# Optimization experiments

Measured on AMD Instinct MI355X. Metric: run time of the kernel, lower is better.

The kernel has to match this reference:

```python
import jax, jax.numpy as jnp
import numpy as np

VOCAB = 267735
CUTOFFS = [20000, 40000, 200000, VOCAB]  # self.cutoffs (incl. vocab)
SHORTLIST = 20000
N_CLUSTERS = 3


def setup_inputs() -> dict:
    key = jax.random.key(0)
    ks = jax.random.split(key, 16)
    s = 0.02  # init scale as in reset_parameters / linear_weight_init
    return {
        "x": jax.random.normal(ks[0], (1024, 1024), jnp.float32),
        "target": jax.random.randint(ks[1], (1024,), 0, VOCAB, jnp.int64),
        "W0": s * jax.random.normal(ks[2], (20000, 1024), jnp.float32),
        "b0": jnp.zeros((20000,), jnp.float32),
        "W1": s * jax.random.normal(ks[3], (20000, 256), jnp.float32),
        "b1": jnp.zeros((20000,), jnp.float32),
        "W2": s * jax.random.normal(ks[4], (160000, 64), jnp.float32),
        "b2": jnp.zeros((160000,), jnp.float32),
        "W3": s * jax.random.normal(ks[5], (67735, 16), jnp.float32),
        "b3": jnp.zeros((67735,), jnp.float32),
        "cluster_weight": s * jax.random.normal(ks[6], (3, 1024), jnp.float32),
        "cluster_bias": jnp.zeros((3,), jnp.float32),
        "P0": s * jax.random.normal(ks[7], (1024, 1024), jnp.float32),
        "P1": s * jax.random.normal(ks[8], (1024, 256), jnp.float32),
        "P2": s * jax.random.normal(ks[9], (1024, 64), jnp.float32),
        "P3": s * jax.random.normal(ks[10], (1024, 16), jnp.float32),
    }


def _logits(x, P, W, b):
    # F.linear(hidden, proj.t()) == x @ proj ; then F.linear(proj_hid, W, b)
    return (x @ P) @ W.T + b


def reference(x, target, W0, b0, W1, b1, W2, b2, W3, b3,
              cluster_weight, cluster_bias, P0, P1, P2, P3):
    N = x.shape[0]
    # head: shortlist + cluster logits
    head_w = jnp.concatenate([W0, cluster_weight], axis=0)  # [20003, 1024]
    head_b = jnp.concatenate([b0, cluster_bias], axis=0)
    head_logp = jax.nn.log_softmax(_logits(x, P0, head_w, head_b), axis=-1)

    # remap targets falling in tail clusters to their cluster token in the head
    # cluster idx -> head index SHORTLIST + N_CLUSTERS - 1 - idx
    head_idx = target
    for idx in range(N_CLUSTERS):
        l, r = CUTOFFS[idx], CUTOFFS[idx + 1]
        in_c = (target >= l) & (target < r)
        head_idx = jnp.where(in_c, SHORTLIST + N_CLUSTERS - 1 - idx, head_idx)

    nll = -jnp.take_along_axis(head_logp, head_idx[:, None], axis=1)[:, 0]

    # tail clusters: dense masked cross-entropy (same math as gather/scatter
    # version: each token contributes only its own cluster's CE)
    tails = [(W1, b1, P1), (W2, b2, P2), (W3, b3, P3)]
    for idx, (W, b, P) in enumerate(tails):
        l, r = CUTOFFS[idx], CUTOFFS[idx + 1]
        mask = (target >= l) & (target < r)
        t = jnp.clip(target - l, 0, r - l - 1)
        logp = jax.nn.log_softmax(_logits(x, P, W, b), axis=-1)  # [N, r-l]
        ce = -jnp.take_along_axis(logp, t[:, None], axis=1)[:, 0]
        nll = nll + jnp.where(mask, ce, jnp.zeros_like(ce))
    return nll
```

## Files before the change

### kernel.cpp

```cpp
#include <hip/hip_runtime.h>
#include <hip/hip_bf16.h>
#include <math.h>


typedef __attribute__((ext_vector_type(4))) float f32x4;
typedef __attribute__((ext_vector_type(8))) short bf16x8;
typedef __attribute__((ext_vector_type(8))) unsigned short ushort8;

#define NEG_INF (-INFINITY)

static __device__ __forceinline__ unsigned short f2b(float f) {
  unsigned u = __builtin_bit_cast(unsigned, f);
  u += 0x7fffu + ((u >> 16) & 1u);
  return (unsigned short)(u >> 16);
}
static __device__ __forceinline__ f32x4 zero4() { f32x4 z = {0.f,0.f,0.f,0.f}; return z; }
static __device__ __forceinline__ ushort8 zero8() { ushort8 z = {0,0,0,0,0,0,0,0}; return z; }

__global__ __launch_bounds__(512, 2)
void gemm_proj(const float* __restrict__ A, const unsigned short* __restrict__ B,
               int V, int K,
               float* __restrict__ Cf, unsigned short* __restrict__ Cb)
{
  __shared__ unsigned short As[256 * 40];
  __shared__ unsigned short Bs[128 * 40];

  const int t = threadIdx.x;
  const int rowBase = blockIdx.y * 256;
  const int colBase = blockIdx.x * 128;

  const int ar = t >> 1, ak = (t & 1) << 4;
  const int br = t >> 2, bk = (t & 3) << 3;
  const bool bval = (colBase + br) < V;
  const size_t arow = (size_t)(rowBase + ar) * K;
  const size_t brow = (size_t)(colBase + br) * K;

  f32x4 aS[4]; ushort8 bSb;
  auto LOAD = [&](int k0) {
    #pragma unroll
    for (int i = 0; i < 4; ++i) aS[i] = *(const f32x4*)(A + arow + k0 + ak + i * 4);
    bSb = bval ? *(const ushort8*)(B + brow + k0 + bk) : zero8();
  };
  auto STORE = [&]() {
    ushort8 p0, p1;
    #pragma unroll
    for (int j = 0; j < 4; ++j) {
      p0[j] = f2b(aS[0][j]); p0[j + 4] = f2b(aS[1][j]);
      p1[j] = f2b(aS[2][j]); p1[j + 4] = f2b(aS[3][j]);
    }
    *(ushort8*)&As[ar * 40 + ak]     = p0;
    *(ushort8*)&As[ar * 40 + ak + 8] = p1;
    *(ushort8*)&Bs[br * 40 + bk] = bSb;
  };

  const int lane = t & 63, w = t >> 6;
  const int wr = w >> 1, wc = w & 1;
  const int g = lane >> 4, fr = lane & 15;

  f32x4 acc[4][4];
  #pragma unroll
  for (int m = 0; m < 4; ++m)
    #pragma unroll
    for (int n = 0; n < 4; ++n) acc[m][n] = zero4();

  LOAD(0);
  for (int k0 = 0; k0 < K; k0 += 32) {
    __syncthreads();
    STORE();
    __syncthreads();
    if (k0 + 32 < K) LOAD(k0 + 32);
    bf16x8 af[4], bf[4];
    #pragma unroll
    for (int m = 0; m < 4; ++m)
      af[m] = *(const bf16x8*)&As[(wr * 64 + m * 16 + fr) * 40 + g * 8];
    #pragma unroll
    for (int n = 0; n < 4; ++n)
      bf[n] = *(const bf16x8*)&Bs[(wc * 64 + n * 16 + fr) * 40 + g * 8];
    #pragma unroll
    for (int m = 0; m < 4; ++m)
      #pragma unroll
      for (int n = 0; n < 4; ++n)
        acc[m][n] = __builtin_amdgcn_mfma_f32_16x16x32_bf16(af[m], bf[n], acc[m][n], 0, 0, 0);
  }

  #pragma unroll
  for (int m = 0; m < 4; ++m) {
    int row = rowBase + wr * 64 + m * 16 + g * 4;
    #pragma unroll
    for (int n = 0; n < 4; ++n) {
      int col = colBase + wc * 64 + n * 16 + fr;
      if (col < V) {
        #pragma unroll
        for (int r = 0; r < 4; ++r) {
          float v = acc[m][n][r];
          Cf[(size_t)(row + r) * V + col] = v;
          Cb[(size_t)(row + r) * V + col] = f2b(v);
        }
      }
    }
  }
}

__global__ __launch_bounds__(512, 2)
void gemm_lse_big(const unsigned short* __restrict__ A, const float* __restrict__ B,
                  const float* __restrict__ bias, int V, int K, int T,
                  float* __restrict__ parts)
{
  __shared__ unsigned short As[256 * 40];
  __shared__ unsigned short Bs[128 * 40];
  __shared__ float red[2][256];

  const int t = threadIdx.x;
  const int rowBase = blockIdx.y * 256;
  const int strip = blockIdx.x;
  const int KS = K >> 5;

  const int ar = t >> 1, ak = (t & 1) << 4;
  const int br = t >> 2, bk = (t & 3) << 3;
  const size_t arow = (size_t)(rowBase + ar) * K;

  ushort8 aSb[2]; f32x4 bS[2];
  auto LOADA = [&](int k0) {
    aSb[0] = *(const ushort8*)(A + arow + k0 + ak);
    aSb[1] = *(const ushort8*)(A + arow + k0 + ak + 8);
  };
  auto LOADB = [&](int tile, int k0) {
    size_t row = (size_t)(strip * T + tile) * 128 + br;
    bool v = row < (size_t)V;
    bS[0] = v ? *(const f32x4*)(B + row * K + k0 + bk)     : zero4();
    bS[1] = v ? *(const f32x4*)(B + row * K + k0 + bk + 4) : zero4();
  };
  auto STORE = [&]() {
    *(ushort8*)&As[ar * 40 + ak]     = aSb[0];
    *(ushort8*)&As[ar * 40 + ak + 8] = aSb[1];
    ushort8 pb;
    #pragma unroll
    for (int j = 0; j < 4; ++j) { pb[j] = f2b(bS[0][j]); pb[j + 4] = f2b(bS[1][j]); }
    *(ushort8*)&Bs[br * 40 + bk] = pb;
  };

  const int lane = t & 63, w = t >> 6;
  const int wr = w >> 1, wc = w & 1;
  const int g = lane >> 4, fr = lane & 15;

  float S[4][4];
  #pragma unroll
  for (int m = 0; m < 4; ++m)
    #pragma unroll
    for (int r = 0; r < 4; ++r) S[m][r] = 0.f;
  f32x4 acc[4][4];
  #pragma unroll
  for (int m = 0; m < 4; ++m)
    #pragma unroll
    for (int n = 0; n < 4; ++n) acc[m][n] = zero4();

  float bcol[4];
  LOADA(0); LOADB(0, 0);
  int tile = 0, ks = 0;
  const int total = T * KS;
  for (int step = 0; step < total; ++step) {
    __syncthreads();
    STORE();
    __syncthreads();
    if (ks == 0) {
      #pragma unroll
      for (int n = 0; n < 4; ++n) {
        int col = (strip * T + tile) * 128 + wc * 64 + n * 16 + fr;
        bcol[n] = (col < V) ? bias[col] : NEG_INF;
      }
    }
    const bool last = (ks == KS - 1);
    int nt = tile, nk = ks + 1;
    if (nk == KS) { nk = 0; nt++; }
    if (nt < T) { LOADA(nk * 32); LOADB(nt, nk * 32); }
    bf16x8 af[4], bfr[4];
    #pragma unroll
    for (int m = 0; m < 4; ++m)
      af[m] = *(const bf16x8*)&As[(wr * 64 + m * 16 + fr) * 40 + g * 8];
    #pragma unroll
    for (int n = 0; n < 4; ++n)
      bfr[n] = *(const bf16x8*)&Bs[(wc * 64 + n * 16 + fr) * 40 + g * 8];
    #pragma unroll
    for (int m = 0; m < 4; ++m)
      #pragma unroll
      for (int n = 0; n < 4; ++n)
        acc[m][n] = __builtin_amdgcn_mfma_f32_16x16x32_bf16(af[m], bfr[n], acc[m][n], 0, 0, 0);
    if (last) {
      #pragma unroll
      for (int m = 0; m < 4; ++m)
        #pragma unroll
        for (int n = 0; n < 4; ++n)
          #pragma unroll
          for (int r = 0; r < 4; ++r)
            S[m][r] += __expf(acc[m][n][r] + bcol[n]);
      #pragma unroll
      for (int m = 0; m < 4; ++m)
        #pragma unroll
        for (int n = 0; n < 4; ++n) acc[m][n] = zero4();
    }
    tile = nt; ks = nk;
  }

  #pragma unroll
  for (int off = 1; off <= 8; off <<= 1)
    #pragma unroll
    for (int m = 0; m < 4; ++m)
      #pragma unroll
      for (int r = 0; r < 4; ++r) S[m][r] += __shfl_xor(S[m][r], off, 64);
  if (fr == 0) {
    #pragma unroll
    for (int m = 0; m < 4; ++m)
      #pragma unroll
      for (int r = 0; r < 4; ++r) red[wc][wr * 64 + m * 16 + g * 4 + r] = S[m][r];
  }
  __syncthreads();
  if (t < 256) parts[(size_t)strip * 1024 + rowBase + t] = red[0][t] + red[1][t];
}

template<int KT>
__global__ __launch_bounds__(512, 2)
void gemm_lse_small(const unsigned short* __restrict__ A, const float* __restrict__ B,
                    const float* __restrict__ bias, int V, int K, int T,
                    float* __restrict__ parts)
{
  constexpr int PITCH = KT + 8;
  __shared__ unsigned short As[256 * PITCH];
  __shared__ unsigned short Bs[2][128 * PITCH];
  __shared__ float red[2][256];

  const int t = threadIdx.x;
  const int rowBase = blockIdx.y * 256;
  const int strip = blockIdx.x;

  {
    int arr = t >> 1, ak0 = (t & 1) * (KT / 2);
    const unsigned short* ap = A + (size_t)(rowBase + arr) * K;
    #pragma unroll
    for (int i = 0; i < KT / 16; ++i) {
      int k = ak0 + i * 8;
      ushort8 v = (k + 8 <= K) ? *(const ushort8*)(ap + k) : zero8();
      *(ushort8*)&As[arr * PITCH + k] = v;
    }
  }

  const int brr = t >> 2, bk0 = (t & 3) * (KT / 4);
  f32x4 bregf[KT / 16];
  auto BLOAD = [&](int tile) {
    size_t row = (size_t)(strip * T + tile) * 128 + brr;
    bool v = row < (size_t)V;
    #pragma unroll
    for (int i = 0; i < KT / 32; ++i) {
      int k = bk0 + i * 8;
      bool kv = v && (k + 8 <= K);
      bregf[2 * i]     = kv ? *(const f32x4*)(B + row * K + k)     : zero4();
      bregf[2 * i + 1] = kv ? *(const f32x4*)(B + row * K + k + 4) : zero4();
    }
  };
  auto BSTORE = [&](int buf) {
    #pragma unroll
    for (int i = 0; i < KT / 32; ++i) {
      int k = bk0 + i * 8;
      ushort8 p;
      #pragma unroll
      for (int j = 0; j < 4; ++j) {
        p[j]     = f2b(bregf[2 * i][j]);
        p[j + 4] = f2b(bregf[2 * i + 1][j]);
      }
      *(ushort8*)&Bs[buf][brr * PITCH + k] = p;
    }
  };

  const int lane = t & 63, w = t >> 6;
  const int wr = w >> 1, wc = w & 1;
  const int g = lane >> 4, fr = lane & 15;

  float S[4][4];
  #pragma unroll
  for (int m = 0; m < 4; ++m)
    #pragma unroll
    for (int r = 0; r < 4; ++r) S[m][r] = 0.f;

  BLOAD(0); BSTORE(0);
  __syncthreads();

  for (int tile = 0; tile < T; ++tile) {
    float bcol[4];
    #pragma unroll
    for (int n = 0; n < 4; ++n) {
      int col = (strip * T + tile) * 128 + wc * 64 + n * 16 + fr;
      bcol[n] = (col < V) ? bias[col] : NEG_INF;
    }
    if (tile + 1 < T) BLOAD(tile + 1);
    f32x4 acc[4][4];
    #pragma unroll
    for (int m = 0; m < 4; ++m)
      #pragma unroll
      for (int n = 0; n < 4; ++n) acc[m][n] = zero4();
    #pragma unroll
    for (int ksub = 0; ksub < KT / 32; ++ksub) {
      bf16x8 af[4], bfr[4];
      #pragma unroll
      for (int m = 0; m < 4; ++m)
        af[m] = *(const bf16x8*)&As[(wr * 64 + m * 16 + fr) * PITCH + ksub * 32 + g * 8];
      #pragma unroll
      for (int n = 0; n < 4; ++n)
        bfr[n] = *(const bf16x8*)&Bs[tile & 1][(wc * 64 + n * 16 + fr) * PITCH + ksub * 32 + g * 8];
      #pragma unroll
      for (int m = 0; m < 4; ++m)
        #pragma unroll
        for (int n = 0; n < 4; ++n)
          acc[m][n] = __builtin_amdgcn_mfma_f32_16x16x32_bf16(af[m], bfr[n], acc[m][n], 0, 0, 0);
    }
    #pragma unroll
    for (int m = 0; m < 4; ++m)
      #pragma unroll
      for (int n = 0; n < 4; ++n)
        #pragma unroll
        for (int r = 0; r < 4; ++r)
          S[m][r] += __expf(acc[m][n][r] + bcol[n]);
    if (tile + 1 < T) BSTORE((tile + 1) & 1);
    __syncthreads();
  }

  #pragma unroll
  for (int off = 1; off <= 8; off <<= 1)
    #pragma unroll
    for (int m = 0; m < 4; ++m)
      #pragma unroll
      for (int r = 0; r < 4; ++r) S[m][r] += __shfl_xor(S[m][r], off, 64);
  if (fr == 0) {
    #pragma unroll
    for (int m = 0; m < 4; ++m)
      #pragma unroll
      for (int r = 0; r < 4; ++r) red[wc][wr * 64 + m * 16 + g * 4 + r] = S[m][r];
  }
  __syncthreads();
  if (t < 256) parts[(size_t)strip * 1024 + rowBase + t] = red[0][t] + red[1][t];
}

__global__ void transpose_k(const float* __restrict__ P, unsigned short* __restrict__ PT, int N)
{
  __shared__ float tile[32][33];
  int tx = threadIdx.x, ty = threadIdx.y;
  int n0 = blockIdx.x * 32, k0 = blockIdx.y * 32;
  #pragma unroll
  for (int j = 0; j < 32; j += 8) {
    int n = n0 + tx;
    tile[ty + j][tx] = (n < N) ? P[(size_t)(k0 + ty + j) * N + n] : 0.f;
  }
  __syncthreads();
  #pragma unroll
  for (int j = 0; j < 32; j += 8) {
    int n = n0 + ty + j;
    if (n < N) PT[(size_t)n * 1024 + (k0 + tx)] = f2b(tile[tx][ty + j]);
  }
}

__global__ void cluster_logits_k(const float* __restrict__ H0,
                                 const float* __restrict__ CW,
                                 const float* __restrict__ cb,
                                 float* __restrict__ clog)
{
  int wid = (blockIdx.x * blockDim.x + threadIdx.x) >> 6;
  int lane = threadIdx.x & 63;
  if (wid >= 1024) return;
  float s0 = 0.f, s1 = 0.f, s2 = 0.f;
  for (int k = lane * 4; k < 1024; k += 256) {
    f32x4 h  = *(const f32x4*)&H0[(size_t)wid * 1024 + k];
    f32x4 w0 = *(const f32x4*)&CW[k];
    f32x4 w1 = *(const f32x4*)&CW[1024 + k];
    f32x4 w2 = *(const f32x4*)&CW[2048 + k];
    #pragma unroll
    for (int j = 0; j < 4; ++j) { s0 += h[j]*w0[j]; s1 += h[j]*w1[j]; s2 += h[j]*w2[j]; }
  }
  #pragma unroll
  for (int off = 1; off <= 32; off <<= 1) {
    s0 += __shfl_xor(s0, off, 64);
    s1 += __shfl_xor(s1, off, 64);
    s2 += __shfl_xor(s2, off, 64);
  }
  if (lane == 0) {
    clog[wid * 3 + 0] = s0 + cb[0];
    clog[wid * 3 + 1] = s1 + cb[1];
    clog[wid * 3 + 2] = s2 + cb[2];
  }
}

__global__ void head_target_k(const float* __restrict__ H0,
                              const float* __restrict__ W0,
                              const float* __restrict__ b0,
                              const float* __restrict__ clog,
                              const int* __restrict__ target,
                              float* __restrict__ headT)
{
  int wid = (blockIdx.x * blockDim.x + threadIdx.x) >> 6;
  int lane = threadIdx.x & 63;
  if (wid >= 1024) return;
  int tg = target[wid];
  if (tg < 20000) {
    const float* wrow = W0 + (size_t)tg * 1024;
    float s = 0.f;
    for (int k = lane * 4; k < 1024; k += 256) {
      f32x4 h = *(const f32x4*)&H0[(size_t)wid * 1024 + k];
      f32x4 v = *(const f32x4*)&wrow[k];
      #pragma unroll
      for (int j = 0; j < 4; ++j) s += h[j] * v[j];
    }
    #pragma unroll
    for (int off = 1; off <= 32; off <<= 1) s += __shfl_xor(s, off, 64);
    if (lane == 0) headT[wid] = s + b0[tg];
  } else if (lane == 0) {
    int idx = (tg < 40000) ? 0 : (tg < 200000) ? 1 : 2;
    headT[wid] = clog[wid * 3 + (2 - idx)];
  }
}

__global__ void tail_target_k(const float* __restrict__ H1, const float* __restrict__ H2,
                              const float* __restrict__ H3,
                              const float* __restrict__ W1, const float* __restrict__ b1,
                              const float* __restrict__ W2, const float* __restrict__ b2,
                              const float* __restrict__ W3, const float* __restrict__ b3,
                              const int* __restrict__ target, float* __restrict__ tailT)
{
  int wid = (blockIdx.x * blockDim.x + threadIdx.x) >> 6;
  int lane = threadIdx.x & 63;
  if (wid >= 1024) return;
  int tg = target[wid];
  if (tg < 20000) { if (lane == 0) tailT[wid] = 0.f; return; }
  const float *H, *W, *bb; int Kc, l;
  if (tg < 40000)       { H = H1; W = W1; bb = b1; Kc = 256; l = 20000; }
  else if (tg < 200000) { H = H2; W = W2; bb = b2; Kc = 64;  l = 40000; }
  else                  { H = H3; W = W3; bb = b3; Kc = 16;  l = 200000; }
  int tt = tg - l;
  float s = 0.f;
  for (int k = lane * 4; k < Kc; k += 256) {
    f32x4 h = *(const f32x4*)&H[(size_t)wid * Kc + k];
    f32x4 v = *(const f32x4*)&W[(size_t)tt * Kc + k];
    #pragma unroll
    for (int j = 0; j < 4; ++j) s += h[j] * v[j];
  }
  #pragma unroll
  for (int off = 1; off <= 32; off <<= 1) s += __shfl_xor(s, off, 64);
  if (lane == 0) tailT[wid] = s + bb[tt];
}

__global__ void finalize_all(const float* __restrict__ parts,
                             const float* __restrict__ clog,
                             const float* __restrict__ headT,
                             const float* __restrict__ tailT,
                             const int* __restrict__ target,
                             float* __restrict__ out)
{
  int wid = (blockIdx.x * blockDim.x + threadIdx.x) >> 6;
  int lane = threadIdx.x & 63;
  if (wid >= 1024) return;
  float s1 = 0.f;
  for (int i = lane; i < 79; i += 64) s1 += parts[(size_t)i * 1024 + wid];
  if (lane < 3) s1 += __expf(clog[wid * 3 + lane]);
  int tg = target[wid];
  float s2 = 0.f;
  if (tg >= 20000) {
    const float* pT; int ns;
    if (tg < 40000)       { pT = parts + (size_t)79  * 1024; ns = 79;  }
    else if (tg < 200000) { pT = parts + (size_t)158 * 1024; ns = 250; }
    else                  { pT = parts + (size_t)408 * 1024; ns = 106; }
    for (int i = lane; i < ns; i += 64) s2 += pT[(size_t)i * 1024 + wid];
  }
  #pragma unroll
  for (int off = 1; off <= 32; off <<= 1) {
    s1 += __shfl_xor(s1, off, 64);
    s2 += __shfl_xor(s2, off, 64);
  }
  if (lane == 0) {
    float nll = logf(s1) - headT[wid];
    if (tg >= 20000) nll += logf(s2) - tailT[wid];
    out[wid] = nll;
  }
}

extern "C" void kernel_launch(void* const* d_in, const int* in_sizes, int n_in,
                              void* d_out, int out_size, void* d_ws, size_t ws_size,
                              hipStream_t stream)
{
  const float* x   = (const float*)d_in[0];
  const int*   tgt = (const int*)d_in[1];
  const float* W0  = (const float*)d_in[2];
  const float* b0  = (const float*)d_in[3];
  const float* W1  = (const float*)d_in[4];
  const float* b1  = (const float*)d_in[5];
  const float* W2  = (const float*)d_in[6];
  const float* b2  = (const float*)d_in[7];
  const float* W3  = (const float*)d_in[8];
  const float* b3  = (const float*)d_in[9];
  const float* CW  = (const float*)d_in[10];
  const float* cb  = (const float*)d_in[11];
  const float* P0  = (const float*)d_in[12];
  const float* P1  = (const float*)d_in[13];
  const float* P2  = (const float*)d_in[14];
  const float* P3  = (const float*)d_in[15];
  float* out = (float*)d_out;

  char* ws = (char*)d_ws;
  size_t off = 0;
  auto alloc = [&](size_t bytes) -> void* {
    void* p = ws + off;
    off = (off + bytes + 255) & ~(size_t)255;
    return p;
  };
  unsigned short* PT0 = (unsigned short*)alloc((size_t)1024 * 1024 * 2);
  unsigned short* PT1 = (unsigned short*)alloc((size_t)256 * 1024 * 2);
  unsigned short* PT2 = (unsigned short*)alloc((size_t)64 * 1024 * 2);
  unsigned short* PT3 = (unsigned short*)alloc((size_t)16 * 1024 * 2);
  float* H0f = (float*)alloc((size_t)1024 * 1024 * 4);
  float* H1f = (float*)alloc((size_t)1024 * 256 * 4);
  float* H2f = (float*)alloc((size_t)1024 * 64 * 4);
  float* H3f = (float*)alloc((size_t)1024 * 16 * 4);
  unsigned short* H0b = (unsigned short*)alloc((size_t)1024 * 1024 * 2);
  unsigned short* H1b = (unsigned short*)alloc((size_t)1024 * 256 * 2);
  unsigned short* H2b = (unsigned short*)alloc((size_t)1024 * 64 * 2);
  unsigned short* H3b = (unsigned short*)alloc((size_t)1024 * 16 * 2);
  float* parts = (float*)alloc((size_t)514 * 1024 * 4);
  float* clog  = (float*)alloc((size_t)1024 * 3 * 4);
  float* headT = (float*)alloc((size_t)1024 * 4);
  float* tailT = (float*)alloc((size_t)1024 * 4);

  float* pHead = parts;
  float* pT1   = parts + (size_t)79  * 1024;
  float* pT2   = parts + (size_t)158 * 1024;
  float* pT3   = parts + (size_t)408 * 1024;

  dim3 tb(32, 8);
  transpose_k<<<dim3(32, 32), tb, 0, stream>>>(P0, PT0, 1024);
  transpose_k<<<dim3(8, 32),  tb, 0, stream>>>(P1, PT1, 256);
  transpose_k<<<dim3(2, 32),  tb, 0, stream>>>(P2, PT2, 64);
  transpose_k<<<dim3(1, 32),  tb, 0, stream>>>(P3, PT3, 16);

  gemm_proj<<<dim3(8, 4), 512, 0, stream>>>(x, PT0, 1024, 1024, H0f, H0b);
  gemm_proj<<<dim3(2, 4), 512, 0, stream>>>(x, PT1, 256,  1024, H1f, H1b);
  gemm_proj<<<dim3(1, 4), 512, 0, stream>>>(x, PT2, 64,   1024, H2f, H2b);
  gemm_proj<<<dim3(1, 4), 512, 0, stream>>>(x, PT3, 16,   1024, H3f, H3b);

  cluster_logits_k<<<256, 256, 0, stream>>>(H0f, CW, cb, clog);
  head_target_k<<<256, 256, 0, stream>>>(H0f, W0, b0, clog, tgt, headT);
  tail_target_k<<<256, 256, 0, stream>>>(H1f, H2f, H3f, W1, b1, W2, b2, W3, b3, tgt, tailT);

  gemm_lse_big<<<dim3(79, 4),  512, 0, stream>>>(H0b, W0, b0, 20000,  1024, 2, pHead);
  gemm_lse_big<<<dim3(79, 4),  512, 0, stream>>>(H1b, W1, b1, 20000,  256,  2, pT1);
  gemm_lse_small<64><<<dim3(250, 4), 512, 0, stream>>>(H2b, W2, b2, 160000, 64, 5, pT2);
  gemm_lse_small<32><<<dim3(106, 4), 512, 0, stream>>>(H3b, W3, b3, 67735,  16, 5, pT3);

  finalize_all<<<256, 256, 0, stream>>>(parts, clog, headT, tailT, tgt, out);
}
```

Baseline: 611.3 us.

## Unify LSE GEMMs into one 128x128-tile kernel with 256-thread blocks

Replaces the big and small LSE GEMM kernels with one generic gemm_lse kernel that uses 128x128 output tiles, 256 threads and K-bounds-checked loads. The projection GEMM also moves to 128-row tiles with 256 threads. Grids grow (e.g. 157x8 and 625x8 blocks), and the partial-sum buffer and finalize indexing are enlarged to match. The aim is more blocks in flight and higher occupancy. The cost is that each W row is now re-read from memory by 8 row-blocks instead of 4, there are more partial sums to reduce, and the small-K path loses its dedicated double buffering.

```diff
diff --git a/kernel.cpp b/kernel.cpp
--- a/kernel.cpp
+++ b/kernel.cpp
@@ -17,29 +17,157 @@
 static __device__ __forceinline__ f32x4 zero4() { f32x4 z = {0.f,0.f,0.f,0.f}; return z; }
 static __device__ __forceinline__ ushort8 zero8() { ushort8 z = {0,0,0,0,0,0,0,0}; return z; }
 
-__global__ __launch_bounds__(512, 2)
+__global__ __launch_bounds__(256, 3)
+void gemm_lse(const unsigned short* __restrict__ A, const float* __restrict__ B,
+              const float* __restrict__ bias, int V, int K, int T,
+              float* __restrict__ parts)
+{
+  __shared__ unsigned short As[128 * 40];
+  __shared__ unsigned short Bs[128 * 40];
+  __shared__ float red[2][128];
+
+  const int t = threadIdx.x;
+  const int rowBase = blockIdx.y * 128;
+  const int strip = blockIdx.x;
+  const int KS = (K + 31) >> 5;
+
+  const int ar = t >> 1, ak = (t & 1) << 4;
+  const int br = t >> 1, bk = (t & 1) << 4;
+  const size_t arow = (size_t)(rowBase + ar) * K;
+
+  ushort8 aSb[2]; f32x4 bS[4];
+  auto LOADB = [&](int tile, int k0) {
+    size_t row = (size_t)(strip * T + tile) * 128 + br;
+    bool v = row < (size_t)V;
+    const float* bp = B + row * (size_t)K;
+    #pragma unroll
+    for (int i = 0; i < 4; ++i) {
+      int k = k0 + bk + i * 4;
+      bS[i] = (v && (k + 4 <= K)) ? *(const f32x4*)(bp + k) : zero4();
+    }
+  };
+  auto LOADA = [&](int k0) {
+    #pragma unroll
+    for (int i = 0; i < 2; ++i) {
+      int k = k0 + ak + i * 8;
+      aSb[i] = (k + 8 <= K) ? *(const ushort8*)(A + arow + k) : zero8();
+    }
+  };
+  auto STORE = [&]() {
+    *(ushort8*)&As[ar * 40 + ak]     = aSb[0];
+    *(ushort8*)&As[ar * 40 + ak + 8] = aSb[1];
+    ushort8 p0, p1;
+    #pragma unroll
+    for (int j = 0; j < 4; ++j) {
+      p0[j] = f2b(bS[0][j]); p0[j + 4] = f2b(bS[1][j]);
+      p1[j] = f2b(bS[2][j]); p1[j + 4] = f2b(bS[3][j]);
+    }
+    *(ushort8*)&Bs[br * 40 + bk]     = p0;
+    *(ushort8*)&Bs[br * 40 + bk + 8] = p1;
+  };
+
+  const int lane = t & 63, w = t >> 6;
+  const int wr = w >> 1, wc = w & 1;
+  const int g = lane >> 4, fr = lane & 15;
+
+  float S[4][4];
+  #pragma unroll
+  for (int m = 0; m < 4; ++m)
+    #pragma unroll
+    for (int r = 0; r < 4; ++r) S[m][r] = 0.f;
+  f32x4 acc[4][4];
+  #pragma unroll
+  for (int m = 0; m < 4; ++m)
+    #pragma unroll
+    for (int n = 0; n < 4; ++n) acc[m][n] = zero4();
+
+  float bcol[4];
+  LOADB(0, 0); LOADA(0);
+  int tile = 0, ks = 0;
+  const int total = T * KS;
+  for (int step = 0; step < total; ++step) {
+    __syncthreads();
+    STORE();
+    __syncthreads();
+    if (ks == 0) {
+      #pragma unroll
+      for (int n = 0; n < 4; ++n) {
+        int col = (strip * T + tile) * 128 + wc * 64 + n * 16 + fr;
+        bcol[n] = (col < V) ? bias[col] : NEG_INF;
+      }
+    }
+    const bool last = (ks == KS - 1);
+    int nt = tile, nk = ks + 1;
+    if (nk == KS) { nk = 0; nt++; }
+    if (nt < T) { LOADB(nt, nk * 32); LOADA(nk * 32); }
+    bf16x8 af[4], bfr[4];
+    #pragma unroll
+    for (int m = 0; m < 4; ++m)
+      af[m] = *(const bf16x8*)&As[(wr * 64 + m * 16 + fr) * 40 + g * 8];
+    #pragma unroll
+    for (int n = 0; n < 4; ++n)
+      bfr[n] = *(const bf16x8*)&Bs[(wc * 64 + n * 16 + fr) * 40 + g * 8];
+    #pragma unroll
+    for (int m = 0; m < 4; ++m)
+      #pragma unroll
+      for (int n = 0; n < 4; ++n)
+        acc[m][n] = __builtin_amdgcn_mfma_f32_16x16x32_bf16(af[m], bfr[n], acc[m][n], 0, 0, 0);
+    if (last) {
+      #pragma unroll
+      for (int m = 0; m < 4; ++m)
+        #pragma unroll
+        for (int n = 0; n < 4; ++n)
+          #pragma unroll
+          for (int r = 0; r < 4; ++r)
+            S[m][r] += __expf(acc[m][n][r] + bcol[n]);
+      #pragma unroll
+      for (int m = 0; m < 4; ++m)
+        #pragma unroll
+        for (int n = 0; n < 4; ++n) acc[m][n] = zero4();
+    }
+    tile = nt; ks = nk;
+  }
+
+  #pragma unroll
+  for (int off = 1; off <= 8; off <<= 1)
+    #pragma unroll
+    for (int m = 0; m < 4; ++m)
+      #pragma unroll
+      for (int r = 0; r < 4; ++r) S[m][r] += __shfl_xor(S[m][r], off, 64);
+  if (fr == 0) {
+    #pragma unroll
+    for (int m = 0; m < 4; ++m)
+      #pragma unroll
+      for (int r = 0; r < 4; ++r) red[wc][wr * 64 + m * 16 + g * 4 + r] = S[m][r];
+  }
+  __syncthreads();
+  if (t < 128) parts[(size_t)strip * 1024 + rowBase + t] = red[0][t] + red[1][t];
+}
+
+__global__ __launch_bounds__(256, 3)
 void gemm_proj(const float* __restrict__ A, const unsigned short* __restrict__ B,
                int V, int K,
                float* __restrict__ Cf, unsigned short* __restrict__ Cb)
 {
-  __shared__ unsigned short As[256 * 40];
+  __shared__ unsigned short As[128 * 40];
   __shared__ unsigned short Bs[128 * 40];
 
   const int t = threadIdx.x;
-  const int rowBase = blockIdx.y * 256;
+  const int rowBase = blockIdx.y * 128;
   const int colBase = blockIdx.x * 128;
 
   const int ar = t >> 1, ak = (t & 1) << 4;
-  const int br = t >> 2, bk = (t & 3) << 3;
+  const int br = t >> 1, bk = (t & 1) << 4;
   const bool bval = (colBase + br) < V;
   const size_t arow = (size_t)(rowBase + ar) * K;
   const size_t brow = (size_t)(colBase + br) * K;
 
-  f32x4 aS[4]; ushort8 bSb;
+  f32x4 aS[4]; ushort8 bSb[2];
   auto LOAD = [&](int k0) {
     #pragma unroll
     for (int i = 0; i < 4; ++i) aS[i] = *(const f32x4*)(A + arow + k0 + ak + i * 4);
-    bSb = bval ? *(const ushort8*)(B + brow + k0 + bk) : zero8();
+    bSb[0] = bval ? *(const ushort8*)(B + brow + k0 + bk)     : zero8();
+    bSb[1] = bval ? *(const ushort8*)(B + brow + k0 + bk + 8) : zero8();
   };
   auto STORE = [&]() {
     ushort8 p0, p1;
@@ -50,7 +178,8 @@
     }
     *(ushort8*)&As[ar * 40 + ak]     = p0;
     *(ushort8*)&As[ar * 40 + ak + 8] = p1;
-    *(ushort8*)&Bs[br * 40 + bk] = bSb;
+    *(ushort8*)&Bs[br * 40 + bk]     = bSb[0];
+    *(ushort8*)&Bs[br * 40 + bk + 8] = bSb[1];
   };
 
   const int lane = t & 63, w = t >> 6;
@@ -69,18 +198,18 @@
     STORE();
     __syncthreads();
     if (k0 + 32 < K) LOAD(k0 + 32);
-    bf16x8 af[4], bf[4];
+    bf16x8 af[4], bfr[4];
     #pragma unroll
     for (int m = 0; m < 4; ++m)
       af[m] = *(const bf16x8*)&As[(wr * 64 + m * 16 + fr) * 40 + g * 8];
     #pragma unroll
     for (int n = 0; n < 4; ++n)
-      bf[n] = *(const bf16x8*)&Bs[(wc * 64 + n * 16 + fr) * 40 + g * 8];
+      bfr[n] = *(const bf16x8*)&Bs[(wc * 64 + n * 16 + fr) * 40 + g * 8];
     #pragma unroll
     for (int m = 0; m < 4; ++m)
       #pragma unroll
       for (int n = 0; n < 4; ++n)
-        acc[m][n] = __builtin_amdgcn_mfma_f32_16x16x32_bf16(af[m], bf[n], acc[m][n], 0, 0, 0);
+        acc[m][n] = __builtin_amdgcn_mfma_f32_16x16x32_bf16(af[m], bfr[n], acc[m][n], 0, 0, 0);
   }
 
   #pragma unroll
@@ -99,243 +228,6 @@
       }
     }
   }
-}
-
-__global__ __launch_bounds__(512, 2)
-void gemm_lse_big(const unsigned short* __restrict__ A, const float* __restrict__ B,
-                  const float* __restrict__ bias, int V, int K, int T,
-                  float* __restrict__ parts)
-{
-  __shared__ unsigned short As[256 * 40];
-  __shared__ unsigned short Bs[128 * 40];
-  __shared__ float red[2][256];
-
-  const int t = threadIdx.x;
-  const int rowBase = blockIdx.y * 256;
-  const int strip = blockIdx.x;
-  const int KS = K >> 5;
-
-  const int ar = t >> 1, ak = (t & 1) << 4;
-  const int br = t >> 2, bk = (t & 3) << 3;
-  const size_t arow = (size_t)(rowBase + ar) * K;
-
-  ushort8 aSb[2]; f32x4 bS[2];
-  auto LOADA = [&](int k0) {
-    aSb[0] = *(const ushort8*)(A + arow + k0 + ak);
-    aSb[1] = *(const ushort8*)(A + arow + k0 + ak + 8);
-  };
-  auto LOADB = [&](int tile, int k0) {
-    size_t row = (size_t)(strip * T + tile) * 128 + br;
-    bool v = row < (size_t)V;
-    bS[0] = v ? *(const f32x4*)(B + row * K + k0 + bk)     : zero4();
-    bS[1] = v ? *(const f32x4*)(B + row * K + k0 + bk + 4) : zero4();
-  };
-  auto STORE = [&]() {
-    *(ushort8*)&As[ar * 40 + ak]     = aSb[0];
-    *(ushort8*)&As[ar * 40 + ak + 8] = aSb[1];
-    ushort8 pb;
-    #pragma unroll
-    for (int j = 0; j < 4; ++j) { pb[j] = f2b(bS[0][j]); pb[j + 4] = f2b(bS[1][j]); }
-    *(ushort8*)&Bs[br * 40 + bk] = pb;
-  };
-
-  const int lane = t & 63, w = t >> 6;
-  const int wr = w >> 1, wc = w & 1;
-  const int g = lane >> 4, fr = lane & 15;
-
-  float S[4][4];
-  #pragma unroll
-  for (int m = 0; m < 4; ++m)
-    #pragma unroll
-    for (int r = 0; r < 4; ++r) S[m][r] = 0.f;
-  f32x4 acc[4][4];
-  #pragma unroll
-  for (int m = 0; m < 4; ++m)
-    #pragma unroll
-    for (int n = 0; n < 4; ++n) acc[m][n] = zero4();
-
-  float bcol[4];
-  LOADA(0); LOADB(0, 0);
-  int tile = 0, ks = 0;
-  const int total = T * KS;
-  for (int step = 0; step < total; ++step) {
-    __syncthreads();
-    STORE();
-    __syncthreads();
-    if (ks == 0) {
-      #pragma unroll
-      for (int n = 0; n < 4; ++n) {
-        int col = (strip * T + tile) * 128 + wc * 64 + n * 16 + fr;
-        bcol[n] = (col < V) ? bias[col] : NEG_INF;
-      }
-    }
-    const bool last = (ks == KS - 1);
-    int nt = tile, nk = ks + 1;
-    if (nk == KS) { nk = 0; nt++; }
-    if (nt < T) { LOADA(nk * 32); LOADB(nt, nk * 32); }
-    bf16x8 af[4], bfr[4];
-    #pragma unroll
-    for (int m = 0; m < 4; ++m)
-      af[m] = *(const bf16x8*)&As[(wr * 64 + m * 16 + fr) * 40 + g * 8];
-    #pragma unroll
-    for (int n = 0; n < 4; ++n)
-      bfr[n] = *(const bf16x8*)&Bs[(wc * 64 + n * 16 + fr) * 40 + g * 8];
-    #pragma unroll
-    for (int m = 0; m < 4; ++m)
-      #pragma unroll
-      for (int n = 0; n < 4; ++n)
-        acc[m][n] = __builtin_amdgcn_mfma_f32_16x16x32_bf16(af[m], bfr[n], acc[m][n], 0, 0, 0);
-    if (last) {
-      #pragma unroll
-      for (int m = 0; m < 4; ++m)
-        #pragma unroll
-        for (int n = 0; n < 4; ++n)
-          #pragma unroll
-          for (int r = 0; r < 4; ++r)
-            S[m][r] += __expf(acc[m][n][r] + bcol[n]);
-      #pragma unroll
-      for (int m = 0; m < 4; ++m)
-        #pragma unroll
-        for (int n = 0; n < 4; ++n) acc[m][n] = zero4();
-    }
-    tile = nt; ks = nk;
-  }
-
-  #pragma unroll
-  for (int off = 1; off <= 8; off <<= 1)
-    #pragma unroll
-    for (int m = 0; m < 4; ++m)
-      #pragma unroll
-      for (int r = 0; r < 4; ++r) S[m][r] += __shfl_xor(S[m][r], off, 64);
-  if (fr == 0) {
-    #pragma unroll
-    for (int m = 0; m < 4; ++m)
-      #pragma unroll
-      for (int r = 0; r < 4; ++r) red[wc][wr * 64 + m * 16 + g * 4 + r] = S[m][r];
-  }
-  __syncthreads();
-  if (t < 256) parts[(size_t)strip * 1024 + rowBase + t] = red[0][t] + red[1][t];
-}
-
-template<int KT>
-__global__ __launch_bounds__(512, 2)
-void gemm_lse_small(const unsigned short* __restrict__ A, const float* __restrict__ B,
-                    const float* __restrict__ bias, int V, int K, int T,
-                    float* __restrict__ parts)
-{
-  constexpr int PITCH = KT + 8;
-  __shared__ unsigned short As[256 * PITCH];
-  __shared__ unsigned short Bs[2][128 * PITCH];
-  __shared__ float red[2][256];
-
-  const int t = threadIdx.x;
-  const int rowBase = blockIdx.y * 256;
-  const int strip = blockIdx.x;
-
-  {
-    int arr = t >> 1, ak0 = (t & 1) * (KT / 2);
-    const unsigned short* ap = A + (size_t)(rowBase + arr) * K;
-    #pragma unroll
-    for (int i = 0; i < KT / 16; ++i) {
-      int k = ak0 + i * 8;
-      ushort8 v = (k + 8 <= K) ? *(const ushort8*)(ap + k) : zero8();
-      *(ushort8*)&As[arr * PITCH + k] = v;
-    }
-  }
-
-  const int brr = t >> 2, bk0 = (t & 3) * (KT / 4);
-  f32x4 bregf[KT / 16];
-  auto BLOAD = [&](int tile) {
-    size_t row = (size_t)(strip * T + tile) * 128 + brr;
-    bool v = row < (size_t)V;
-    #pragma unroll
-    for (int i = 0; i < KT / 32; ++i) {
-      int k = bk0 + i * 8;
-      bool kv = v && (k + 8 <= K);
-      bregf[2 * i]     = kv ? *(const f32x4*)(B + row * K + k)     : zero4();
-      bregf[2 * i + 1] = kv ? *(const f32x4*)(B + row * K + k + 4) : zero4();
-    }
-  };
-  auto BSTORE = [&](int buf) {
-    #pragma unroll
-    for (int i = 0; i < KT / 32; ++i) {
-      int k = bk0 + i * 8;
-      ushort8 p;
-      #pragma unroll
-      for (int j = 0; j < 4; ++j) {
-        p[j]     = f2b(bregf[2 * i][j]);
-        p[j + 4] = f2b(bregf[2 * i + 1][j]);
-      }
-      *(ushort8*)&Bs[buf][brr * PITCH + k] = p;
-    }
-  };
-
-  const int lane = t & 63, w = t >> 6;
-  const int wr = w >> 1, wc = w & 1;
-  const int g = lane >> 4, fr = lane & 15;
-
-  float S[4][4];
-  #pragma unroll
-  for (int m = 0; m < 4; ++m)
-    #pragma unroll
-    for (int r = 0; r < 4; ++r) S[m][r] = 0.f;
-
-  BLOAD(0); BSTORE(0);
-  __syncthreads();
-
-  for (int tile = 0; tile < T; ++tile) {
-    float bcol[4];
-    #pragma unroll
-    for (int n = 0; n < 4; ++n) {
-      int col = (strip * T + tile) * 128 + wc * 64 + n * 16 + fr;
-      bcol[n] = (col < V) ? bias[col] : NEG_INF;
-    }
-    if (tile + 1 < T) BLOAD(tile + 1);
-    f32x4 acc[4][4];
-    #pragma unroll
-    for (int m = 0; m < 4; ++m)
-      #pragma unroll
-      for (int n = 0; n < 4; ++n) acc[m][n] = zero4();
-    #pragma unroll
-    for (int ksub = 0; ksub < KT / 32; ++ksub) {
-      bf16x8 af[4], bfr[4];
-      #pragma unroll
-      for (int m = 0; m < 4; ++m)
-        af[m] = *(const bf16x8*)&As[(wr * 64 + m * 16 + fr) * PITCH + ksub * 32 + g * 8];
-      #pragma unroll
-      for (int n = 0; n < 4; ++n)
-        bfr[n] = *(const bf16x8*)&Bs[tile & 1][(wc * 64 + n * 16 + fr) * PITCH + ksub * 32 + g * 8];
-      #pragma unroll
-      for (int m = 0; m < 4; ++m)
-        #pragma unroll
-        for (int n = 0; n < 4; ++n)
-          acc[m][n] = __builtin_amdgcn_mfma_f32_16x16x32_bf16(af[m], bfr[n], acc[m][n], 0, 0, 0);
-    }
-    #pragma unroll
-    for (int m = 0; m < 4; ++m)
-      #pragma unroll
-      for (int n = 0; n < 4; ++n)
-        #pragma unroll
-        for (int r = 0; r < 4; ++r)
-          S[m][r] += __expf(acc[m][n][r] + bcol[n]);
-    if (tile + 1 < T) BSTORE((tile + 1) & 1);
-    __syncthreads();
-  }
-
-  #pragma unroll
-  for (int off = 1; off <= 8; off <<= 1)
-    #pragma unroll
-    for (int m = 0; m < 4; ++m)
-      #pragma unroll
-      for (int r = 0; r < 4; ++r) S[m][r] += __shfl_xor(S[m][r], off, 64);
-  if (fr == 0) {
-    #pragma unroll
-    for (int m = 0; m < 4; ++m)
-      #pragma unroll
-      for (int r = 0; r < 4; ++r) red[wc][wr * 64 + m * 16 + g * 4 + r] = S[m][r];
-  }
-  __syncthreads();
-  if (t < 256) parts[(size_t)strip * 1024 + rowBase + t] = red[0][t] + red[1][t];
 }
 
 __global__ void transpose_k(const float* __restrict__ P, unsigned short* __restrict__ PT, int N)
@@ -455,15 +347,15 @@
   int lane = threadIdx.x & 63;
   if (wid >= 1024) return;
   float s1 = 0.f;
-  for (int i = lane; i < 79; i += 64) s1 += parts[(size_t)i * 1024 + wid];
+  for (int i = lane; i < 157; i += 64) s1 += parts[(size_t)i * 1024 + wid];
   if (lane < 3) s1 += __expf(clog[wid * 3 + lane]);
   int tg = target[wid];
   float s2 = 0.f;
   if (tg >= 20000) {
     const float* pT; int ns;
-    if (tg < 40000)       { pT = parts + (size_t)79  * 1024; ns = 79;  }
-    else if (tg < 200000) { pT = parts + (size_t)158 * 1024; ns = 250; }
-    else                  { pT = parts + (size_t)408 * 1024; ns = 106; }
+    if (tg < 40000)       { pT = parts + (size_t)157 * 1024; ns = 157; }
+    else if (tg < 200000) { pT = parts + (size_t)314 * 1024; ns = 625; }
+    else                  { pT = parts + (size_t)939 * 1024; ns = 265; }
     for (int i = lane; i < ns; i += 64) s2 += pT[(size_t)i * 1024 + wid];
   }
   #pragma unroll
@@ -519,15 +411,15 @@
   unsigned short* H1b = (unsigned short*)alloc((size_t)1024 * 256 * 2);
   unsigned short* H2b = (unsigned short*)alloc((size_t)1024 * 64 * 2);
   unsigned short* H3b = (unsigned short*)alloc((size_t)1024 * 16 * 2);
-  float* parts = (float*)alloc((size_t)514 * 1024 * 4);
+  float* parts = (float*)alloc((size_t)1204 * 1024 * 4);
   float* clog  = (float*)alloc((size_t)1024 * 3 * 4);
   float* headT = (float*)alloc((size_t)1024 * 4);
   float* tailT = (float*)alloc((size_t)1024 * 4);
 
   float* pHead = parts;
-  float* pT1   = parts + (size_t)79  * 1024;
-  float* pT2   = parts + (size_t)158 * 1024;
-  float* pT3   = parts + (size_t)408 * 1024;
+  float* pT1   = parts + (size_t)157 * 1024;
+  float* pT2   = parts + (size_t)314 * 1024;
+  float* pT3   = parts + (size_t)939 * 1024;
 
   dim3 tb(32, 8);
   transpose_k<<<dim3(32, 32), tb, 0, stream>>>(P0, PT0, 1024);
@@ -535,19 +427,19 @@
   transpose_k<<<dim3(2, 32),  tb, 0, stream>>>(P2, PT2, 64);
   transpose_k<<<dim3(1, 32),  tb, 0, stream>>>(P3, PT3, 16);
 
-  gemm_proj<<<dim3(8, 4), 512, 0, stream>>>(x, PT0, 1024, 1024, H0f, H0b);
-  gemm_proj<<<dim3(2, 4), 512, 0, stream>>>(x, PT1, 256,  1024, H1f, H1b);
-  gemm_proj<<<dim3(1, 4), 512, 0, stream>>>(x, PT2, 64,   1024, H2f, H2b);
-  gemm_proj<<<dim3(1, 4), 512, 0, stream>>>(x, PT3, 16,   1024, H3f, H3b);
+  gemm_proj<<<dim3(8, 8), 256, 0, stream>>>(x, PT0, 1024, 1024, H0f, H0b);
+  gemm_proj<<<dim3(2, 8), 256, 0, stream>>>(x, PT1, 256,  1024, H1f, H1b);
+  gemm_proj<<<dim3(1, 8), 256, 0, stream>>>(x, PT2, 64,   1024, H2f, H2b);
+  gemm_proj<<<dim3(1, 8), 256, 0, stream>>>(x, PT3, 16,   1024, H3f, H3b);
 
   cluster_logits_k<<<256, 256, 0, stream>>>(H0f, CW, cb, clog);
   head_target_k<<<256, 256, 0, stream>>>(H0f, W0, b0, clog, tgt, headT);
   tail_target_k<<<256, 256, 0, stream>>>(H1f, H2f, H3f, W1, b1, W2, b2, W3, b3, tgt, tailT);
 
-  gemm_lse_big<<<dim3(79, 4),  512, 0, stream>>>(H0b, W0, b0, 20000,  1024, 2, pHead);
-  gemm_lse_big<<<dim3(79, 4),  512, 0, stream>>>(H1b, W1, b1, 20000,  256,  2, pT1);
-  gemm_lse_small<64><<<dim3(250, 4), 512, 0, stream>>>(H2b, W2, b2, 160000, 64, 5, pT2);
-  gemm_lse_small<32><<<dim3(106, 4), 512, 0, stream>>>(H3b, W3, b3, 67735,  16, 5, pT3);
+  gemm_lse<<<dim3(157, 8), 256, 0, stream>>>(H0b, W0, b0, 20000,  1024, 1, pHead);
+  gemm_lse<<<dim3(157, 8), 256, 0, stream>>>(H1b, W1, b1, 20000,  256,  1, pT1);
+  gemm_lse<<<dim3(625, 8), 256, 0, stream>>>(H2b, W2, b2, 160000, 64,   2, pT2);
+  gemm_lse<<<dim3(265, 8), 256, 0, stream>>>(H3b, W3, b3, 67735,  16,   2, pT3);
 
   finalize_all<<<256, 256, 0, stream>>>(parts, clog, headT, tailT, tgt, out);
 }
```

After: 559.3 us. 8.5% less time.
